# Kernel tuning notes

Hardware: AMD Instinct MI355X
Metric: run time of the kernel (lower is better)

## Reference

```python
import jax, jax.numpy as jnp
import numpy as np

N_NODES = 100000
N_EDGES = 3200000
NUM_TYPES = 8
TYPE_DIM = 16
IN_DIM = 5
HID = 64
HEADS = 2
OUT = 64
LN_EPS = 1e-5
NEG_SLOPE = 0.2


def segment_softmax(logits, seg, num_segments):
    # logits: [E, H], seg: [E] destination ids
    m = jax.ops.segment_max(logits, seg, num_segments=num_segments)
    m = jnp.where(jnp.isfinite(m), m, 0.0)
    e = jnp.exp(logits - m[seg])
    s = jax.ops.segment_sum(e, seg, num_segments=num_segments)
    return e / (s[seg] + 1e-16)


def gat_conv(x, W, a_src, a_dst, b, src, dst, n_nodes, heads, ch):
    # x: [N, F_in], W: [F_in, heads*ch], a_src/a_dst: [heads, ch], b: [heads*ch]
    h = (x @ W).reshape(n_nodes, heads, ch)            # [N, H, C]
    al_s = jnp.einsum('nhc,hc->nh', h, a_src)          # [N, H]
    al_d = jnp.einsum('nhc,hc->nh', h, a_dst)          # [N, H]
    e = jax.nn.leaky_relu(al_s[src] + al_d[dst], NEG_SLOPE)  # [E, H]
    alpha = segment_softmax(e, dst, n_nodes)           # [E, H]
    msg = alpha[:, :, None] * h[src]                   # [E, H, C]
    out = jax.ops.segment_sum(msg, dst, num_segments=n_nodes)  # [N, H, C]
    return out.reshape(n_nodes, heads * ch) + b


def setup_inputs() -> dict:
    key = jax.random.key(0)
    ks = jax.random.split(key, 16)
    in1 = IN_DIM + TYPE_DIM  # 21
    inp = {
        'x': jax.random.normal(ks[0], (N_NODES, IN_DIM), dtype=jnp.float32),
        'edge_index': jax.random.randint(ks[1], (2, N_EDGES), 0, N_NODES, dtype=jnp.int32),
        'type_ids': jax.random.randint(ks[2], (N_NODES,), 0, NUM_TYPES, dtype=jnp.int32),
        'type_emb': jax.random.normal(ks[3], (NUM_TYPES, TYPE_DIM), dtype=jnp.float32) * 0.3,
        'W1': jax.random.normal(ks[4], (in1, HID), dtype=jnp.float32) * (1.0 / np.sqrt(in1)),
        'a_src1': jax.random.normal(ks[5], (HEADS, HID // HEADS), dtype=jnp.float32) * 0.1,
        'a_dst1': jax.random.normal(ks[6], (HEADS, HID // HEADS), dtype=jnp.float32) * 0.1,
        'b1': jnp.zeros((HID,), dtype=jnp.float32),
        'W2': jax.random.normal(ks[7], (HID, OUT), dtype=jnp.float32) * (1.0 / np.sqrt(HID)),
        'a_src2': jax.random.normal(ks[8], (1, OUT), dtype=jnp.float32) * 0.1,
        'a_dst2': jax.random.normal(ks[9], (1, OUT), dtype=jnp.float32) * 0.1,
        'b2': jnp.zeros((OUT,), dtype=jnp.float32),
        'gamma': jnp.ones((OUT,), dtype=jnp.float32),
        'beta': jnp.zeros((OUT,), dtype=jnp.float32),
    }
    return inp


def reference(x, type_emb, W1, a_src1, a_dst1, b1, W2, a_src2, a_dst2, b2, gamma, beta, edge_index, type_ids):
    n = x.shape[0]
    # type embedding concat
    xin = jnp.concatenate([x, type_emb[type_ids]], axis=1)  # [N, 21]
    # add self loops (PyG GATConv default)
    loops = jnp.arange(n, dtype=edge_index.dtype)
    src = jnp.concatenate([edge_index[0], loops])
    dst = jnp.concatenate([edge_index[1], loops])
    h = gat_conv(xin, W1, a_src1, a_dst1, b1, src, dst, n, HEADS, HID // HEADS)
    h = jax.nn.relu(h)  # dropout = identity at inference
    h = gat_conv(h, W2, a_src2, a_dst2, b2, src, dst, n, 1, OUT)
    # LayerNorm
    mu = jnp.mean(h, axis=-1, keepdims=True)
    var = jnp.var(h, axis=-1, keepdims=True)
    return (h - mu) / jnp.sqrt(var + LN_EPS) * gamma + beta
```

## Files before the change

### kernel.cpp

```cpp
#include <hip/hip_runtime.h>
#include <hip/hip_fp16.h>

#define NEG_SLOPE 0.2f
#define BKT_SHIFT 8
#define BKT_NODES 256
#define BKT_CAP 10240
#define SRC_SHIFT 18
#define SRC_MASK 0x3FFFF
#define CHUNK 8192
#define NBMAX 512

typedef _Float16 half8 __attribute__((ext_vector_type(8)));
typedef float float4v __attribute__((ext_vector_type(4)));

__device__ __forceinline__ int wave_iscan(int v, int lane) {
#pragma unroll
    for (int off = 1; off < 64; off <<= 1) {
        int u = __shfl_up(v, off);
        if (lane >= off) v += u;
    }
    return v;
}

__global__ __launch_bounds__(512) void k_fat(
        const float* __restrict__ x, const int* __restrict__ type_ids,
        const float* __restrict__ type_emb, const float* __restrict__ W1,
        const float* __restrict__ a_src1, const float* __restrict__ a_dst1,
        __half2* __restrict__ h1h, float* __restrict__ als1, float* __restrict__ ald1,
        const int* __restrict__ ei, unsigned int* __restrict__ pk,
        int* __restrict__ bcnt, int E, int NBKT, int N)
{
    __shared__ unsigned int stage[CHUNK];
    __shared__ unsigned short stageB[CHUNK];
    __shared__ int cnt[NBMAX];
    __shared__ int excl[NBMAX];
    __shared__ int curp[NBMAX];
    __shared__ int gbase[NBMAX];
    __shared__ int wpart[8];

    int t = threadIdx.x;
    if (blockIdx.x < (unsigned)NBKT) {
        int lane = t & 63, wv = t >> 6;
        int e0 = blockIdx.x * CHUNK;
        bool vec4 = ((E & 3) == 0);

        cnt[t] = 0;
        __syncthreads();

        int4 s4[4], d4[4];
        bool val[4];

        if (vec4) {
#pragma unroll
            for (int it = 0; it < 4; it++) {
                int e = e0 + it * 2048 + t * 4;
                val[it] = (e < E);
                if (val[it]) {
                    s4[it] = *(const int4*)(ei + e);
                    d4[it] = *(const int4*)(ei + (size_t)E + e);
                    atomicAdd(&cnt[d4[it].x >> BKT_SHIFT], 1);
                    atomicAdd(&cnt[d4[it].y >> BKT_SHIFT], 1);
                    atomicAdd(&cnt[d4[it].z >> BKT_SHIFT], 1);
                    atomicAdd(&cnt[d4[it].w >> BKT_SHIFT], 1);
                }
            }
        } else {
            for (int i = t; i < CHUNK; i += 512) {
                int e = e0 + i;
                if (e >= E) break;
                atomicAdd(&cnt[ei[E + e] >> BKT_SHIFT], 1);
            }
        }
        __syncthreads();
        int myc = cnt[t];
        int incl = wave_iscan(myc, lane);
        if (lane == 63) wpart[wv] = incl;
        __syncthreads();
#pragma unroll
        for (int k = 0; k < 8; k++)
            if (k < wv) incl += wpart[k];
        {
            int ex = incl - myc;
            excl[t] = ex;
            curp[t] = ex;
            if (t < NBKT)
                gbase[t] = (myc > 0) ? atomicAdd(&bcnt[t], myc) : 0;
        }
        __syncthreads();
        if (vec4) {
#pragma unroll
            for (int it = 0; it < 4; it++) {
                if (!val[it]) continue;
                int ss[4] = {s4[it].x, s4[it].y, s4[it].z, s4[it].w};
                int dd[4] = {d4[it].x, d4[it].y, d4[it].z, d4[it].w};
#pragma unroll
                for (int k = 0; k < 4; k++) {
                    int b = dd[k] >> BKT_SHIFT;
                    int p = atomicAdd(&curp[b], 1);
                    stage[p] = (unsigned)ss[k] | ((unsigned)(dd[k] & (BKT_NODES - 1)) << SRC_SHIFT);
                    stageB[p] = (unsigned short)b;
                }
            }
        } else {
            for (int i = t; i < CHUNK; i += 512) {
                int e = e0 + i;
                if (e >= E) break;
                int s = ei[e], d = ei[E + e];
                int b = d >> BKT_SHIFT;
                int p = atomicAdd(&curp[b], 1);
                stage[p] = (unsigned)s | ((unsigned)(d & (BKT_NODES - 1)) << SRC_SHIFT);
                stageB[p] = (unsigned short)b;
            }
        }
        __syncthreads();
        int total = E - e0; if (total > CHUNK) total = CHUNK;
        for (int i = t; i < total; i += 512) {
            int b = stageB[i];
            int idx = gbase[b] + (i - excl[b]);
            if (idx < BKT_CAP) pk[(size_t)b * BKT_CAP + idx] = stage[i];
        }
    } else {
        int node = (blockIdx.x - NBKT) * 8 + (t >> 6);
        int j = t & 63;
        if (node >= N) return;

        float xin[21];
#pragma unroll
        for (int k = 0; k < 5; k++) xin[k] = x[node * 5 + k];
        int ty = type_ids[node];
#pragma unroll
        for (int k = 0; k < 16; k++) xin[5 + k] = type_emb[ty * 16 + k];

        float h = 0.f;
#pragma unroll
        for (int k = 0; k < 21; k++) h += xin[k] * W1[k * 64 + j];

        float hn = __shfl_xor(h, 1);
        if ((j & 1) == 0)
            h1h[node * 32 + (j >> 1)] = __floats2half2_rn(h, hn);

        int head = j >> 5, lane = j & 31;
        float ps = h * a_src1[head * 32 + lane];
        float pd = h * a_dst1[head * 32 + lane];
#pragma unroll
        for (int m = 16; m >= 1; m >>= 1) { ps += __shfl_xor(ps, m); pd += __shfl_xor(pd, m); }
        if (lane == 0) { als1[node * 2 + head] = ps; ald1[node * 2 + head] = pd; }
    }
}

__global__ __launch_bounds__(512) void k_gbsm1(
        const unsigned int* __restrict__ pk, const int* __restrict__ bcnt,
        const float4* __restrict__ h4, const float* __restrict__ als1,
        const float* __restrict__ ald1, const float* __restrict__ b1,
        const float* __restrict__ W2, const float* __restrict__ a_src2,
        const float* __restrict__ a_dst2,
        int* __restrict__ rs, int* __restrict__ cur, int* __restrict__ ssrc,
        _Float16* __restrict__ h3h, float* __restrict__ als2,
        float* __restrict__ ald2, int N)
{
    __shared__ int cnt[BKT_NODES];
    __shared__ int cursor[BKT_NODES];
    __shared__ int nodebeg[BKT_NODES];
    __shared__ int red[512];
    __shared__ int wpart[4];
    __shared__ _Float16 h2t[BKT_NODES][72];
    __shared__ _Float16 w2t[64][72];

    int b = blockIdx.x;
    int t = threadIdx.x;
    int lane = t & 63, wv = t >> 6;
    int nb = min(bcnt[b], BKT_CAP);
    int nbase = b << BKT_SHIFT;
    int nn = min(BKT_NODES, N - nbase);

    for (int e = t; e < 4096; e += 512) {
        int kk = e >> 6, nc = e & 63;
        w2t[nc][kk] = (_Float16)W2[e];
    }

    int part = 0;
    for (int i2 = t; i2 < b; i2 += 512) part += min(bcnt[i2], BKT_CAP);
    red[t] = part;
    if (t < BKT_NODES) cnt[t] = 0;
    __syncthreads();
    for (int off = 256; off; off >>= 1) {
        if (t < off) red[t] += red[t + off];
        __syncthreads();
    }
    int bs = red[0];

    const unsigned int* mypk = pk + (size_t)b * BKT_CAP;
    int nb4 = nb & ~3;
    for (int e = t * 4; e < nb4; e += 2048) {
        uint4 v = *(const uint4*)(mypk + e);
        atomicAdd(&cnt[v.x >> SRC_SHIFT], 1);
        atomicAdd(&cnt[v.y >> SRC_SHIFT], 1);
        atomicAdd(&cnt[v.z >> SRC_SHIFT], 1);
        atomicAdd(&cnt[v.w >> SRC_SHIFT], 1);
    }
    for (int e = nb4 + t; e < nb; e += 512) {
        atomicAdd(&cnt[mypk[e] >> SRC_SHIFT], 1);
    }
    __syncthreads();
    if (t < BKT_NODES) {
        int myc = cnt[t];
        int incl = wave_iscan(myc, lane);
        if (lane == 63) wpart[wv] = incl;
        __syncthreads();
#pragma unroll
        for (int k = 0; k < 4; k++)
            if (k < wv) incl += wpart[k];
        int ex = incl - myc;
        cursor[t] = ex;
        nodebeg[t] = bs + ex;
        int node = nbase + t;
        if (node < N) { rs[node] = bs + ex; cur[node] = bs + ex + myc; }
    } else {
        __syncthreads();
    }
    __syncthreads();
    for (int e = t; e < nb; e += 512) {
        unsigned int w = mypk[e];
        int p = atomicAdd(&cursor[w >> SRC_SHIFT], 1);
        ssrc[bs + p] = (int)(w & SRC_MASK);
    }
    __syncthreads();

    int l = t & 63;
    int q = l & 15, i = q & 7, hlf = q >> 3;
    int grpbase = l & 48;
    int head = i >> 2;
    int g = t >> 4;

    for (int ln = g; ln < BKT_NODES; ln += 32) {
        bool live = ln < nn;
        int lnc = live ? ln : (nn - 1);
        int node = nbase + lnc;
        int beg = nodebeg[lnc];
        int cnt_n = live ? cnt[lnc] : 0;

        float ad0 = ald1[node * 2 + 0];
        float ad1 = ald1[node * 2 + 1];
        float ad = head ? ad1 : ad0;

        int mc = cnt_n;
        mc = max(mc, __shfl_xor(mc, 16));
        mc = max(mc, __shfl_xor(mc, 32));

        float acc[8];
#pragma unroll
        for (int k = 0; k < 8; k++) acc[k] = 0.f;
        float wsum = 0.f;

        for (int bb = 0; bb < mc; bb += 16) {
            int slot = bb + q;
            bool valid = slot < cnt_n;
            int idx = valid ? (beg + slot) : 0;
            int s = ssrc[idx];
            if (!valid) s = node;
            float2 al = *(const float2*)(als1 + (size_t)s * 2);
            float lg0 = al.x + ad0; lg0 = (lg0 >= 0.f) ? lg0 : NEG_SLOPE * lg0;
            float lg1 = al.y + ad1; lg1 = (lg1 >= 0.f) ? lg1 : NEG_SLOPE * lg1;
            float w0 = valid ? __expf(lg0) : 0.f;
            float w1 = valid ? __expf(lg1) : 0.f;
            __half2 wp = __floats2half2_rn(w0, w1);
            unsigned wpi = *(unsigned*)&wp;

#pragma unroll
            for (int r = 0; r < 8; r++) {
                int srcl = grpbase + hlf * 8 + r;
                int sr = __shfl(s, srcl);
                unsigned wri = __shfl(wpi, srcl);
                __half2 wh = *(__half2*)&wri;
                float w = head ? __high2float(wh) : __low2float(wh);
                float4 rv = h4[(size_t)sr * 8 + i];
                const __half* hp = (const __half*)&rv;
#pragma unroll
                for (int k = 0; k < 8; k++)
                    acc[k] = fmaf(w, __half2float(hp[k]), acc[k]);
                wsum += w;
            }
        }

#pragma unroll
        for (int k = 0; k < 8; k++) acc[k] += __shfl_xor(acc[k], 8);
        wsum += __shfl_xor(wsum, 8);

        {
            float lg = als1[node * 2 + head] + ad;
            lg = (lg >= 0.f) ? lg : NEG_SLOPE * lg;
            float w = __expf(lg);
            float4 rv = h4[(size_t)node * 8 + i];
            const __half* hp = (const __half*)&rv;
#pragma unroll
            for (int k = 0; k < 8; k++)
                acc[k] = fmaf(w, __half2float(hp[k]), acc[k]);
            wsum += w;
        }

        float inv = 1.f / (wsum + 1e-16f);
        if (hlf == 0) {
            union { float4 f4; __half2 h2[4]; } u;
#pragma unroll
            for (int c4 = 0; c4 < 4; c4++) {
                float v0 = fmaxf(acc[2*c4]   * inv + b1[i * 8 + 2*c4],     0.f);
                float v1 = fmaxf(acc[2*c4+1] * inv + b1[i * 8 + 2*c4 + 1], 0.f);
                u.h2[c4] = __floats2half2_rn(v0, v1);
            }
            *(float4*)(&h2t[ln][i * 8]) = u.f4;
        }
    }
    __syncthreads();

    int l15 = lane & 15, quad = lane >> 4;
#pragma unroll
    for (int rti = 0; rti < 2; rti++) {
        int rt = wv * 2 + rti;
        half8 a0 = *(const half8*)(&h2t[rt * 16 + l15][quad * 8]);
        half8 a1 = *(const half8*)(&h2t[rt * 16 + l15][32 + quad * 8]);
        float4v accs[4];
#pragma unroll
        for (int ct = 0; ct < 4; ct++) {
            half8 bf0 = *(const half8*)(&w2t[ct * 16 + l15][quad * 8]);
            half8 bf1 = *(const half8*)(&w2t[ct * 16 + l15][32 + quad * 8]);
            float4v c = {0.f, 0.f, 0.f, 0.f};
            c = __builtin_amdgcn_mfma_f32_16x16x32_f16(a0, bf0, c, 0, 0, 0);
            c = __builtin_amdgcn_mfma_f32_16x16x32_f16(a1, bf1, c, 0, 0, 0);
            accs[ct] = c;
        }
        float ps[4] = {0.f, 0.f, 0.f, 0.f};
        float pd[4] = {0.f, 0.f, 0.f, 0.f};
#pragma unroll
        for (int ct = 0; ct < 4; ct++) {
            float as = a_src2[ct * 16 + l15];
            float av = a_dst2[ct * 16 + l15];
#pragma unroll
            for (int r = 0; r < 4; r++) {
                ps[r] += accs[ct][r] * as;
                pd[r] += accs[ct][r] * av;
            }
        }
#pragma unroll
        for (int m = 1; m <= 8; m <<= 1) {
#pragma unroll
            for (int r = 0; r < 4; r++) {
                ps[r] += __shfl_xor(ps[r], m);
                pd[r] += __shfl_xor(pd[r], m);
            }
        }
#pragma unroll
        for (int r = 0; r < 4; r++) {
            int row = rt * 16 + quad * 4 + r;
            int node = nbase + row;
            if (node < N) {
                if (l15 == 0) { als2[node] = ps[r]; ald2[node] = pd[r]; }
#pragma unroll
                for (int ct = 0; ct < 4; ct++)
                    h3h[(size_t)node * 64 + ct * 16 + l15] = (_Float16)accs[ct][r];
            }
        }
    }
}

__global__ void k_gather2(const int* __restrict__ rs, const int* __restrict__ cur,
                          const int* __restrict__ ssrc, const float4* __restrict__ h4,
                          const float* __restrict__ als2, const float* __restrict__ ald2,
                          const float* __restrict__ b2, const float* __restrict__ gamma,
                          const float* __restrict__ beta, float* __restrict__ out, int N)
{
    int t = threadIdx.x;
    int l = t & 63;
    int q = l & 15;
    int i = q & 7;
    int hlf = q >> 3;
    int grpbase = l & 48;

    int node = blockIdx.x * 16 + (t >> 4);
    bool live = node < N;
    int node_c = live ? node : (N - 1);

    int beg = rs[node_c];
    int cnt = live ? (cur[node_c] - beg) : 0;
    float ad = ald2[node_c];

    int mc = cnt;
    mc = max(mc, __shfl_xor(mc, 16));
    mc = max(mc, __shfl_xor(mc, 32));

    float acc[8];
#pragma unroll
    for (int k = 0; k < 8; k++) acc[k] = 0.f;
    float wsum = 0.f;

    for (int b = 0; b < mc; b += 16) {
        int slot = b + q;
        bool valid = slot < cnt;
        int idx = valid ? (beg + slot) : 0;
        int s = ssrc[idx];
        if (!valid) s = node_c;
        float lg = als2[s] + ad;
        lg = (lg >= 0.f) ? lg : NEG_SLOPE * lg;
        float w = valid ? __expf(lg) : 0.f;

#pragma unroll
        for (int r = 0; r < 8; r++) {
            int srcl = grpbase + hlf * 8 + r;
            int sr = __shfl(s, srcl);
            float wr = __shfl(w, srcl);
            float4 rv = h4[(size_t)sr * 8 + i];
            const __half* hp = (const __half*)&rv;
#pragma unroll
            for (int k = 0; k < 8; k++)
                acc[k] = fmaf(wr, __half2float(hp[k]), acc[k]);
            wsum += wr;
        }
    }

#pragma unroll
    for (int k = 0; k < 8; k++) acc[k] += __shfl_xor(acc[k], 8);
    wsum += __shfl_xor(wsum, 8);

    {
        float lg = als2[node_c] + ad;
        lg = (lg >= 0.f) ? lg : NEG_SLOPE * lg;
        float w = __expf(lg);
        float4 rv = h4[(size_t)node_c * 8 + i];
        const __half* hp = (const __half*)&rv;
#pragma unroll
        for (int k = 0; k < 8; k++)
            acc[k] = fmaf(w, __half2float(hp[k]), acc[k]);
        wsum += w;
    }

    float inv = 1.f / (wsum + 1e-16f);
    float o[8];
    float s = 0.f;
#pragma unroll
    for (int k = 0; k < 8; k++) { o[k] = acc[k] * inv + b2[i * 8 + k]; s += o[k]; }
    s += __shfl_xor(s, 1); s += __shfl_xor(s, 2); s += __shfl_xor(s, 4);
    float mu = s * (1.f / 64.f);
    float v = 0.f;
#pragma unroll
    for (int k = 0; k < 8; k++) { float d = o[k] - mu; v += d * d; }
    v += __shfl_xor(v, 1); v += __shfl_xor(v, 2); v += __shfl_xor(v, 4);
    v *= (1.f / 64.f);
    float rstd = rsqrtf(v + 1e-5f);
    if (live && hlf == 0) {
        float res[8];
#pragma unroll
        for (int k = 0; k < 8; k++)
            res[k] = (o[k] - mu) * rstd * gamma[i * 8 + k] + beta[i * 8 + k];
        float4* op = (float4*)(out + (size_t)node * 64 + i * 8);
        op[0] = make_float4(res[0], res[1], res[2], res[3]);
        op[1] = make_float4(res[4], res[5], res[6], res[7]);
    }
}

extern "C" void kernel_launch(void* const* d_in, const int* in_sizes, int n_in,
                              void* d_out, int out_size, void* d_ws, size_t ws_size,
                              hipStream_t stream) {
    const float* x        = (const float*)d_in[0];
    const int*   ei       = (const int*)  d_in[1];
    const int*   type_ids = (const int*)  d_in[2];
    const float* type_emb = (const float*)d_in[3];
    const float* W1       = (const float*)d_in[4];
    const float* a_src1   = (const float*)d_in[5];
    const float* a_dst1   = (const float*)d_in[6];
    const float* b1       = (const float*)d_in[7];
    const float* W2       = (const float*)d_in[8];
    const float* a_src2   = (const float*)d_in[9];
    const float* a_dst2   = (const float*)d_in[10];
    const float* b2       = (const float*)d_in[11];
    const float* gamma    = (const float*)d_in[12];
    const float* beta     = (const float*)d_in[13];

    int N = in_sizes[0] / 5;
    int E = in_sizes[1] / 2;
    int NBKT = (N + BKT_NODES - 1) >> BKT_SHIFT;

    char* base = (char*)d_ws;
    size_t off = 0;
    auto carve = [&](size_t bytes) { void* p = base + off; off += (bytes + 255) & ~(size_t)255; return p; };
    __half2* h1h = (__half2*)carve((size_t)N * 64 * sizeof(__half));
    unsigned int* pk = (unsigned int*)carve((size_t)NBKT * BKT_CAP * sizeof(unsigned int));
    _Float16* h3h = (_Float16*)carve((size_t)N * 64 * sizeof(__half));
    float* als1  = (float*)carve((size_t)N * 2 * sizeof(float));
    float* ald1  = (float*)carve((size_t)N * 2 * sizeof(float));
    float* als2  = (float*)carve((size_t)N * sizeof(float));
    float* ald2  = (float*)carve((size_t)N * sizeof(float));
    int*   rs    = (int*)carve((size_t)N * sizeof(int));
    int*   cur   = (int*)carve((size_t)N * sizeof(int));
    int*   bcnt  = (int*)carve(1024 * sizeof(int));
    int*   ssrc  = (int*)carve((size_t)E * sizeof(int) + 256);

    dim3 tb(256);
    dim3 tb512(512);

    hipMemsetAsync(bcnt, 0, NBKT * sizeof(int), stream);

    int nodeblks = (N + 7) / 8;
    k_fat<<<dim3(NBKT + nodeblks), tb512, 0, stream>>>(
        x, type_ids, type_emb, W1, a_src1, a_dst1, h1h, als1, ald1,
        ei, pk, bcnt, E, NBKT, N);

    k_gbsm1<<<dim3(NBKT), tb512, 0, stream>>>(
        pk, bcnt, (const float4*)h1h, als1, ald1, b1,
        W2, a_src2, a_dst2, rs, cur, ssrc, h3h, als2, ald2, N);

    dim3 ng((N + 15) / 16);
    k_gather2<<<ng, tb, 0, stream>>>(rs, cur, ssrc, (const float4*)h3h, als2, ald2, b2,
                                     gamma, beta, (float*)d_out, N);
}
```

Before: 314.5 us.

## Fold node projection into edge-bucketing blocks instead of separate node blocks

Each block of the first kernel now first computes the layer-1 projection and attention logits for 256 nodes, one node per wave per iteration, and then buckets its own chunk of edges. This replaces the old split grid of edge blocks plus many small per-8-node blocks. The grid is sized as the larger of the edge-chunk count and the node-block count, which also decouples the chunk count from the bucket count. The memset now clears the whole bucket-counter buffer. The aim is to cut block-launch and scheduling overhead, at the cost of running node work in series before the edge work inside each block, so there is less independent parallelism across the GPU.

Result: faster. 299.8 us (-4.7%).

```diff
diff --git a/kernel.cpp b/kernel.cpp
--- a/kernel.cpp
+++ b/kernel.cpp
@@ -22,13 +22,13 @@
     return v;
 }
 
-__global__ __launch_bounds__(512) void k_fat(
+__global__ __launch_bounds__(512) void k_bkn1(
         const float* __restrict__ x, const int* __restrict__ type_ids,
         const float* __restrict__ type_emb, const float* __restrict__ W1,
         const float* __restrict__ a_src1, const float* __restrict__ a_dst1,
         __half2* __restrict__ h1h, float* __restrict__ als1, float* __restrict__ ald1,
         const int* __restrict__ ei, unsigned int* __restrict__ pk,
-        int* __restrict__ bcnt, int E, int NBKT, int N)
+        int* __restrict__ bcnt, int E, int NCHUNKS, int NBKT, int N)
 {
     __shared__ unsigned int stage[CHUNK];
     __shared__ unsigned short stageB[CHUNK];
@@ -39,112 +39,115 @@
     __shared__ int wpart[8];
 
     int t = threadIdx.x;
-    if (blockIdx.x < (unsigned)NBKT) {
-        int lane = t & 63, wv = t >> 6;
-        int e0 = blockIdx.x * CHUNK;
-        bool vec4 = ((E & 3) == 0);
-
-        cnt[t] = 0;
-        __syncthreads();
-
-        int4 s4[4], d4[4];
-        bool val[4];
-
-        if (vec4) {
-#pragma unroll
-            for (int it = 0; it < 4; it++) {
-                int e = e0 + it * 2048 + t * 4;
-                val[it] = (e < E);
-                if (val[it]) {
-                    s4[it] = *(const int4*)(ei + e);
-                    d4[it] = *(const int4*)(ei + (size_t)E + e);
-                    atomicAdd(&cnt[d4[it].x >> BKT_SHIFT], 1);
-                    atomicAdd(&cnt[d4[it].y >> BKT_SHIFT], 1);
-                    atomicAdd(&cnt[d4[it].z >> BKT_SHIFT], 1);
-                    atomicAdd(&cnt[d4[it].w >> BKT_SHIFT], 1);
-                }
-            }
-        } else {
-            for (int i = t; i < CHUNK; i += 512) {
-                int e = e0 + i;
-                if (e >= E) break;
-                atomicAdd(&cnt[ei[E + e] >> BKT_SHIFT], 1);
-            }
-        }
-        __syncthreads();
-        int myc = cnt[t];
-        int incl = wave_iscan(myc, lane);
-        if (lane == 63) wpart[wv] = incl;
-        __syncthreads();
-#pragma unroll
-        for (int k = 0; k < 8; k++)
-            if (k < wv) incl += wpart[k];
-        {
-            int ex = incl - myc;
-            excl[t] = ex;
-            curp[t] = ex;
-            if (t < NBKT)
-                gbase[t] = (myc > 0) ? atomicAdd(&bcnt[t], myc) : 0;
-        }
-        __syncthreads();
-        if (vec4) {
-#pragma unroll
-            for (int it = 0; it < 4; it++) {
-                if (!val[it]) continue;
-                int ss[4] = {s4[it].x, s4[it].y, s4[it].z, s4[it].w};
-                int dd[4] = {d4[it].x, d4[it].y, d4[it].z, d4[it].w};
-#pragma unroll
-                for (int k = 0; k < 4; k++) {
-                    int b = dd[k] >> BKT_SHIFT;
-                    int p = atomicAdd(&curp[b], 1);
-                    stage[p] = (unsigned)ss[k] | ((unsigned)(dd[k] & (BKT_NODES - 1)) << SRC_SHIFT);
-                    stageB[p] = (unsigned short)b;
-                }
-            }
-        } else {
-            for (int i = t; i < CHUNK; i += 512) {
-                int e = e0 + i;
-                if (e >= E) break;
-                int s = ei[e], d = ei[E + e];
-                int b = d >> BKT_SHIFT;
+    int lane = t & 63, wv = t >> 6;
+
+    {
+        int nend = min((int)(blockIdx.x + 1) * 256, N);
+        for (int node = blockIdx.x * 256 + wv; node < nend; node += 8) {
+            int j = lane;
+            float xin[21];
+#pragma unroll
+            for (int k = 0; k < 5; k++) xin[k] = x[node * 5 + k];
+            int ty = type_ids[node];
+#pragma unroll
+            for (int k = 0; k < 16; k++) xin[5 + k] = type_emb[ty * 16 + k];
+
+            float h = 0.f;
+#pragma unroll
+            for (int k = 0; k < 21; k++) h += xin[k] * W1[k * 64 + j];
+
+            float hn = __shfl_xor(h, 1);
+            if ((j & 1) == 0)
+                h1h[node * 32 + (j >> 1)] = __floats2half2_rn(h, hn);
+
+            int head = j >> 5, l31 = j & 31;
+            float ps = h * a_src1[head * 32 + l31];
+            float pd = h * a_dst1[head * 32 + l31];
+#pragma unroll
+            for (int m = 16; m >= 1; m >>= 1) { ps += __shfl_xor(ps, m); pd += __shfl_xor(pd, m); }
+            if (l31 == 0) { als1[node * 2 + head] = ps; ald1[node * 2 + head] = pd; }
+        }
+    }
+
+    if (blockIdx.x >= (unsigned)NCHUNKS) return;
+
+    int e0 = blockIdx.x * CHUNK;
+    bool vec4 = ((E & 3) == 0);
+
+    cnt[t] = 0;
+    __syncthreads();
+
+    int4 s4[4], d4[4];
+    bool val[4];
+
+    if (vec4) {
+#pragma unroll
+        for (int it = 0; it < 4; it++) {
+            int e = e0 + it * 2048 + t * 4;
+            val[it] = (e < E);
+            if (val[it]) {
+                s4[it] = *(const int4*)(ei + e);
+                d4[it] = *(const int4*)(ei + (size_t)E + e);
+                atomicAdd(&cnt[d4[it].x >> BKT_SHIFT], 1);
+                atomicAdd(&cnt[d4[it].y >> BKT_SHIFT], 1);
+                atomicAdd(&cnt[d4[it].z >> BKT_SHIFT], 1);
+                atomicAdd(&cnt[d4[it].w >> BKT_SHIFT], 1);
+            }
+        }
+    } else {
+        for (int i = t; i < CHUNK; i += 512) {
+            int e = e0 + i;
+            if (e >= E) break;
+            atomicAdd(&cnt[ei[E + e] >> BKT_SHIFT], 1);
+        }
+    }
+    __syncthreads();
+    int myc = cnt[t];
+    int incl = wave_iscan(myc, lane);
+    if (lane == 63) wpart[wv] = incl;
+    __syncthreads();
+#pragma unroll
+    for (int k = 0; k < 8; k++)
+        if (k < wv) incl += wpart[k];
+    {
+        int ex = incl - myc;
+        excl[t] = ex;
+        curp[t] = ex;
+        if (t < NBKT)
+            gbase[t] = (myc > 0) ? atomicAdd(&bcnt[t], myc) : 0;
+    }
+    __syncthreads();
+    if (vec4) {
+#pragma unroll
+        for (int it = 0; it < 4; it++) {
+            if (!val[it]) continue;
+            int ss[4] = {s4[it].x, s4[it].y, s4[it].z, s4[it].w};
+            int dd[4] = {d4[it].x, d4[it].y, d4[it].z, d4[it].w};
+#pragma unroll
+            for (int k = 0; k < 4; k++) {
+                int b = dd[k] >> BKT_SHIFT;
                 int p = atomicAdd(&curp[b], 1);
-                stage[p] = (unsigned)s | ((unsigned)(d & (BKT_NODES - 1)) << SRC_SHIFT);
+                stage[p] = (unsigned)ss[k] | ((unsigned)(dd[k] & (BKT_NODES - 1)) << SRC_SHIFT);
                 stageB[p] = (unsigned short)b;
             }
         }
-        __syncthreads();
-        int total = E - e0; if (total > CHUNK) total = CHUNK;
-        for (int i = t; i < total; i += 512) {
-            int b = stageB[i];
-            int idx = gbase[b] + (i - excl[b]);
-            if (idx < BKT_CAP) pk[(size_t)b * BKT_CAP + idx] = stage[i];
-        }
     } else {
-        int node = (blockIdx.x - NBKT) * 8 + (t >> 6);
-        int j = t & 63;
-        if (node >= N) return;
-
-        float xin[21];
-#pragma unroll
-        for (int k = 0; k < 5; k++) xin[k] = x[node * 5 + k];
-        int ty = type_ids[node];
-#pragma unroll
-        for (int k = 0; k < 16; k++) xin[5 + k] = type_emb[ty * 16 + k];
-
-        float h = 0.f;
-#pragma unroll
-        for (int k = 0; k < 21; k++) h += xin[k] * W1[k * 64 + j];
-
-        float hn = __shfl_xor(h, 1);
-        if ((j & 1) == 0)
-            h1h[node * 32 + (j >> 1)] = __floats2half2_rn(h, hn);
-
-        int head = j >> 5, lane = j & 31;
-        float ps = h * a_src1[head * 32 + lane];
-        float pd = h * a_dst1[head * 32 + lane];
-#pragma unroll
-        for (int m = 16; m >= 1; m >>= 1) { ps += __shfl_xor(ps, m); pd += __shfl_xor(pd, m); }
-        if (lane == 0) { als1[node * 2 + head] = ps; ald1[node * 2 + head] = pd; }
+        for (int i = t; i < CHUNK; i += 512) {
+            int e = e0 + i;
+            if (e >= E) break;
+            int s = ei[e], d = ei[E + e];
+            int b = d >> BKT_SHIFT;
+            int p = atomicAdd(&curp[b], 1);
+            stage[p] = (unsigned)s | ((unsigned)(d & (BKT_NODES - 1)) << SRC_SHIFT);
+            stageB[p] = (unsigned short)b;
+        }
+    }
+    __syncthreads();
+    int total = E - e0; if (total > CHUNK) total = CHUNK;
+    for (int i = t; i < total; i += 512) {
+        int b = stageB[i];
+        int idx = gbase[b] + (i - excl[b]);
+        if (idx < BKT_CAP) pk[(size_t)b * BKT_CAP + idx] = stage[i];
     }
 }
 
@@ -477,6 +480,7 @@
     int N = in_sizes[0] / 5;
     int E = in_sizes[1] / 2;
     int NBKT = (N + BKT_NODES - 1) >> BKT_SHIFT;
+    int NCHUNKS = (E + CHUNK - 1) / CHUNK;
 
     char* base = (char*)d_ws;
     size_t off = 0;
@@ -496,12 +500,13 @@
     dim3 tb(256);
     dim3 tb512(512);
 
-    hipMemsetAsync(bcnt, 0, NBKT * sizeof(int), stream);
-
-    int nodeblks = (N + 7) / 8;
-    k_fat<<<dim3(NBKT + nodeblks), tb512, 0, stream>>>(
+    hipMemsetAsync(bcnt, 0, 1024 * sizeof(int), stream);
+
+    int nodeblks = (N + 255) / 256;
+    int fatgrid = NCHUNKS > nodeblks ? NCHUNKS : nodeblks;
+    k_bkn1<<<dim3(fatgrid), tb512, 0, stream>>>(
         x, type_ids, type_emb, W1, a_src1, a_dst1, h1h, als1, ald1,
-        ei, pk, bcnt, E, NBKT, N);
+        ei, pk, bcnt, E, NCHUNKS, NBKT, N);
 
     k_gbsm1<<<dim3(NBKT), tb512, 0, stream>>>(
         pk, bcnt, (const float4*)h1h, als1, ald1, b1,
```

## Split fused node/bucket kernel and scatter edges directly without LDS staging

Applied to the files above, without the earlier changes.

The fused kernel, which combined node feature projection with edge bucketing, is split into two kernels: k_node1 and k_bucketA. The bucket kernel drops its LDS staging buffer and prefix scan. Each edge now takes its slot through an LDS atomic cursor seeded from the global bucket base and is written straight to global memory. The separate memset is removed, and bcnt is zeroed by block 0 of the node kernel instead. This cuts LDS use and a barrier phase, but global writes become more scattered and the two phases no longer overlap within one launch.

Measured after the change: 314.9 us. Within noise of the previous version (+0.1%).

```diff
diff --git a/kernel.cpp b/kernel.cpp
--- a/kernel.cpp
+++ b/kernel.cpp
@@ -22,129 +22,116 @@
     return v;
 }
 
-__global__ __launch_bounds__(512) void k_fat(
-        const float* __restrict__ x, const int* __restrict__ type_ids,
-        const float* __restrict__ type_emb, const float* __restrict__ W1,
-        const float* __restrict__ a_src1, const float* __restrict__ a_dst1,
-        __half2* __restrict__ h1h, float* __restrict__ als1, float* __restrict__ ald1,
+__global__ void k_node1(const float* __restrict__ x, const int* __restrict__ type_ids,
+                        const float* __restrict__ type_emb, const float* __restrict__ W1,
+                        const float* __restrict__ a_src1, const float* __restrict__ a_dst1,
+                        __half2* __restrict__ h1h, float* __restrict__ als1, float* __restrict__ ald1,
+                        int* __restrict__ bcnt, int N)
+{
+    if (blockIdx.x == 0) {
+        for (int z = threadIdx.x; z < 1024; z += 256) bcnt[z] = 0;
+    }
+    int node = blockIdx.x * 4 + (threadIdx.x >> 6);
+    int j = threadIdx.x & 63;
+    if (node >= N) return;
+
+    float xin[21];
+#pragma unroll
+    for (int k = 0; k < 5; k++) xin[k] = x[node * 5 + k];
+    int t = type_ids[node];
+#pragma unroll
+    for (int k = 0; k < 16; k++) xin[5 + k] = type_emb[t * 16 + k];
+
+    float h = 0.f;
+#pragma unroll
+    for (int k = 0; k < 21; k++) h += xin[k] * W1[k * 64 + j];
+
+    float hn = __shfl_xor(h, 1);
+    if ((j & 1) == 0)
+        h1h[node * 32 + (j >> 1)] = __floats2half2_rn(h, hn);
+
+    int head = j >> 5, lane = j & 31;
+    float ps = h * a_src1[head * 32 + lane];
+    float pd = h * a_dst1[head * 32 + lane];
+#pragma unroll
+    for (int m = 16; m >= 1; m >>= 1) { ps += __shfl_xor(ps, m); pd += __shfl_xor(pd, m); }
+    if (lane == 0) { als1[node * 2 + head] = ps; ald1[node * 2 + head] = pd; }
+}
+
+__global__ __launch_bounds__(512) void k_bucketA(
         const int* __restrict__ ei, unsigned int* __restrict__ pk,
-        int* __restrict__ bcnt, int E, int NBKT, int N)
+        int* __restrict__ bcnt, int E, int NBKT)
 {
-    __shared__ unsigned int stage[CHUNK];
-    __shared__ unsigned short stageB[CHUNK];
     __shared__ int cnt[NBMAX];
-    __shared__ int excl[NBMAX];
     __shared__ int curp[NBMAX];
-    __shared__ int gbase[NBMAX];
-    __shared__ int wpart[8];
 
     int t = threadIdx.x;
-    if (blockIdx.x < (unsigned)NBKT) {
-        int lane = t & 63, wv = t >> 6;
-        int e0 = blockIdx.x * CHUNK;
-        bool vec4 = ((E & 3) == 0);
-
-        cnt[t] = 0;
-        __syncthreads();
-
-        int4 s4[4], d4[4];
-        bool val[4];
-
-        if (vec4) {
-#pragma unroll
-            for (int it = 0; it < 4; it++) {
-                int e = e0 + it * 2048 + t * 4;
-                val[it] = (e < E);
-                if (val[it]) {
-                    s4[it] = *(const int4*)(ei + e);
-                    d4[it] = *(const int4*)(ei + (size_t)E + e);
-                    atomicAdd(&cnt[d4[it].x >> BKT_SHIFT], 1);
-                    atomicAdd(&cnt[d4[it].y >> BKT_SHIFT], 1);
-                    atomicAdd(&cnt[d4[it].z >> BKT_SHIFT], 1);
-                    atomicAdd(&cnt[d4[it].w >> BKT_SHIFT], 1);
-                }
-            }
-        } else {
-            for (int i = t; i < CHUNK; i += 512) {
-                int e = e0 + i;
-                if (e >= E) break;
-                atomicAdd(&cnt[ei[E + e] >> BKT_SHIFT], 1);
-            }
-        }
-        __syncthreads();
+    int e0 = blockIdx.x * CHUNK;
+    bool vec4 = ((E & 3) == 0);
+
+    cnt[t] = 0;
+    __syncthreads();
+
+    int4 s4[4], d4[4];
+    bool val[4];
+
+    if (vec4) {
+#pragma unroll
+        for (int it = 0; it < 4; it++) {
+            int e = e0 + it * 2048 + t * 4;
+            val[it] = (e < E);
+            if (val[it]) {
+                s4[it] = *(const int4*)(ei + e);
+                d4[it] = *(const int4*)(ei + (size_t)E + e);
+                atomicAdd(&cnt[d4[it].x >> BKT_SHIFT], 1);
+                atomicAdd(&cnt[d4[it].y >> BKT_SHIFT], 1);
+                atomicAdd(&cnt[d4[it].z >> BKT_SHIFT], 1);
+                atomicAdd(&cnt[d4[it].w >> BKT_SHIFT], 1);
+            }
+        }
+    } else {
+        for (int i = t; i < CHUNK; i += 512) {
+            int e = e0 + i;
+            if (e >= E) break;
+            atomicAdd(&cnt[ei[E + e] >> BKT_SHIFT], 1);
+        }
+    }
+    __syncthreads();
+
+    {
         int myc = cnt[t];
-        int incl = wave_iscan(myc, lane);
-        if (lane == 63) wpart[wv] = incl;
-        __syncthreads();
-#pragma unroll
-        for (int k = 0; k < 8; k++)
-            if (k < wv) incl += wpart[k];
-        {
-            int ex = incl - myc;
-            excl[t] = ex;
-            curp[t] = ex;
-            if (t < NBKT)
-                gbase[t] = (myc > 0) ? atomicAdd(&bcnt[t], myc) : 0;
-        }
-        __syncthreads();
-        if (vec4) {
-#pragma unroll
-            for (int it = 0; it < 4; it++) {
-                if (!val[it]) continue;
-                int ss[4] = {s4[it].x, s4[it].y, s4[it].z, s4[it].w};
-                int dd[4] = {d4[it].x, d4[it].y, d4[it].z, d4[it].w};
-#pragma unroll
-                for (int k = 0; k < 4; k++) {
-                    int b = dd[k] >> BKT_SHIFT;
-                    int p = atomicAdd(&curp[b], 1);
-                    stage[p] = (unsigned)ss[k] | ((unsigned)(dd[k] & (BKT_NODES - 1)) << SRC_SHIFT);
-                    stageB[p] = (unsigned short)b;
-                }
-            }
-        } else {
-            for (int i = t; i < CHUNK; i += 512) {
-                int e = e0 + i;
-                if (e >= E) break;
-                int s = ei[e], d = ei[E + e];
-                int b = d >> BKT_SHIFT;
+        int gb = 0;
+        if (t < NBKT && myc > 0) gb = atomicAdd(&bcnt[t], myc);
+        curp[t] = gb;
+    }
+    __syncthreads();
+
+    if (vec4) {
+#pragma unroll
+        for (int it = 0; it < 4; it++) {
+            if (!val[it]) continue;
+            int ss[4] = {s4[it].x, s4[it].y, s4[it].z, s4[it].w};
+            int dd[4] = {d4[it].x, d4[it].y, d4[it].z, d4[it].w};
+#pragma unroll
+            for (int k = 0; k < 4; k++) {
+                int b = dd[k] >> BKT_SHIFT;
                 int p = atomicAdd(&curp[b], 1);
-                stage[p] = (unsigned)s | ((unsigned)(d & (BKT_NODES - 1)) << SRC_SHIFT);
-                stageB[p] = (unsigned short)b;
-            }
-        }
-        __syncthreads();
-        int total = E - e0; if (total > CHUNK) total = CHUNK;
-        for (int i = t; i < total; i += 512) {
-            int b = stageB[i];
-            int idx = gbase[b] + (i - excl[b]);
-            if (idx < BKT_CAP) pk[(size_t)b * BKT_CAP + idx] = stage[i];
+                if (p < BKT_CAP)
+                    pk[(size_t)b * BKT_CAP + p] =
+                        (unsigned)ss[k] | ((unsigned)(dd[k] & (BKT_NODES - 1)) << SRC_SHIFT);
+            }
         }
     } else {
-        int node = (blockIdx.x - NBKT) * 8 + (t >> 6);
-        int j = t & 63;
-        if (node >= N) return;
-
-        float xin[21];
-#pragma unroll
-        for (int k = 0; k < 5; k++) xin[k] = x[node * 5 + k];
-        int ty = type_ids[node];
-#pragma unroll
-        for (int k = 0; k < 16; k++) xin[5 + k] = type_emb[ty * 16 + k];
-
-        float h = 0.f;
-#pragma unroll
-        for (int k = 0; k < 21; k++) h += xin[k] * W1[k * 64 + j];
-
-        float hn = __shfl_xor(h, 1);
-        if ((j & 1) == 0)
-            h1h[node * 32 + (j >> 1)] = __floats2half2_rn(h, hn);
-
-        int head = j >> 5, lane = j & 31;
-        float ps = h * a_src1[head * 32 + lane];
-        float pd = h * a_dst1[head * 32 + lane];
-#pragma unroll
-        for (int m = 16; m >= 1; m >>= 1) { ps += __shfl_xor(ps, m); pd += __shfl_xor(pd, m); }
-        if (lane == 0) { als1[node * 2 + head] = ps; ald1[node * 2 + head] = pd; }
+        for (int i = t; i < CHUNK; i += 512) {
+            int e = e0 + i;
+            if (e >= E) break;
+            int s = ei[e], d = ei[E + e];
+            int b = d >> BKT_SHIFT;
+            int p = atomicAdd(&curp[b], 1);
+            if (p < BKT_CAP)
+                pk[(size_t)b * BKT_CAP + p] =
+                    (unsigned)s | ((unsigned)(d & (BKT_NODES - 1)) << SRC_SHIFT);
+        }
     }
 }
 
@@ -477,6 +464,7 @@
     int N = in_sizes[0] / 5;
     int E = in_sizes[1] / 2;
     int NBKT = (N + BKT_NODES - 1) >> BKT_SHIFT;
+    int NCHUNKS = (E + CHUNK - 1) / CHUNK;
 
     char* base = (char*)d_ws;
     size_t off = 0;
@@ -496,12 +484,10 @@
     dim3 tb(256);
     dim3 tb512(512);
 
-    hipMemsetAsync(bcnt, 0, NBKT * sizeof(int), stream);
-
-    int nodeblks = (N + 7) / 8;
-    k_fat<<<dim3(NBKT + nodeblks), tb512, 0, stream>>>(
-        x, type_ids, type_emb, W1, a_src1, a_dst1, h1h, als1, ald1,
-        ei, pk, bcnt, E, NBKT, N);
+    k_node1<<<dim3((N + 3) / 4), tb, 0, stream>>>(x, type_ids, type_emb, W1, a_src1, a_dst1,
+                                                  h1h, als1, ald1, bcnt, N);
+
+    k_bucketA<<<dim3(NCHUNKS), tb512, 0, stream>>>(ei, pk, bcnt, E, NBKT);
 
     k_gbsm1<<<dim3(NBKT), tb512, 0, stream>>>(
         pk, bcnt, (const float4*)h1h, als1, ald1, b1,
```
